# Kernel tuning notes

Hardware: AMD Instinct MI355X
Metric: run time of the kernel (lower is better)

The kernel has to match this reference:

```python
import jax, jax.numpy as jnp
import numpy as np

DIM = 1024
NUM_HEADS = 16
HEAD_DIM = DIM // NUM_HEADS
THETA = 10000.0


def apply_rope(x):
    # x: [B, S, H, D]; Llama-style interleaved rotary pairs.
    S, D = x.shape[1], x.shape[3]
    half = D // 2
    inv_freq = THETA ** (-jnp.arange(half, dtype=jnp.float32) * 2.0 / D)  # [D/2]
    angles = jnp.arange(S, dtype=jnp.float32)[:, None] * inv_freq[None, :]  # [S, D/2]
    cos = jnp.cos(angles)[None, :, None, :]  # [1,S,1,D/2]
    sin = jnp.sin(angles)[None, :, None, :]
    x_even = x[..., 0::2]
    x_odd = x[..., 1::2]
    out_even = x_even * cos - x_odd * sin
    out_odd = x_even * sin + x_odd * cos
    out = jnp.stack([out_even, out_odd], axis=-1).reshape(x.shape)
    return out.astype(x.dtype)


def setup_inputs() -> dict:
    key = jax.random.key(0)
    ks = jax.random.split(key, 5)
    B, S = 2, 2048
    x = jax.random.normal(ks[0], (B, S, DIM), dtype=jnp.float32)
    scale = 1.0 / np.sqrt(DIM)
    Wq = jax.random.normal(ks[1], (DIM, DIM), dtype=jnp.float32) * scale
    Wk = jax.random.normal(ks[2], (DIM, DIM), dtype=jnp.float32) * scale
    Wv = jax.random.normal(ks[3], (DIM, DIM), dtype=jnp.float32) * scale
    Wo = jax.random.normal(ks[4], (DIM, DIM), dtype=jnp.float32) * scale
    return {"x": x, "Wq": Wq, "Wk": Wk, "Wv": Wv, "Wo": Wo}


def reference(x, Wq, Wk, Wv, Wo):
    B, S, _ = x.shape
    # torch Linear: y = x @ W^T
    q = (x @ Wq.T).reshape(B, S, NUM_HEADS, HEAD_DIM)
    k = (x @ Wk.T).reshape(B, S, NUM_HEADS, HEAD_DIM)
    v = (x @ Wv.T).reshape(B, S, NUM_HEADS, HEAD_DIM)
    q = apply_rope(q)
    k = apply_rope(k)
    # causal SDPA, scale = 1/sqrt(head_dim)
    scale = 1.0 / np.sqrt(HEAD_DIM).astype(np.float32)
    scores = jnp.einsum("bqhd,bkhd->bhqk", q, k) * scale  # [B,H,S,S]
    causal = jnp.tril(jnp.ones((S, S), dtype=bool))
    scores = jnp.where(causal[None, None], scores, jnp.finfo(scores.dtype).min)
    attn = jax.nn.softmax(scores, axis=-1)
    y = jnp.einsum("bhqk,bkhd->bqhd", attn, v).reshape(B, S, DIM)
    return y @ Wo.T
```

## Files before the change

### kernel.cpp

```cpp
#include <hip/hip_runtime.h>
#include <hip/hip_bf16.h>

typedef __attribute__((ext_vector_type(8))) __bf16 bf16x8;
typedef __attribute__((ext_vector_type(4))) __bf16 bf16x4;
typedef __attribute__((ext_vector_type(4))) float f32x4;
typedef __attribute__((ext_vector_type(16))) float f32x16;
typedef __attribute__((ext_vector_type(2))) unsigned int uint2v;
typedef __attribute__((ext_vector_type(4))) unsigned int uint4v;

#define DIM 1024
#define SLEN 2048
#define NH 16
#define HD 64

__device__ __forceinline__ f32x4 MFMA(bf16x8 a, bf16x8 b, f32x4 c) {
    return __builtin_amdgcn_mfma_f32_16x16x32_bf16(a, b, c, 0, 0, 0);
}
__device__ __forceinline__ f32x16 MFMA32(bf16x8 a, bf16x8 b, f32x16 c) {
    return __builtin_amdgcn_mfma_f32_32x32x16_bf16(a, b, c, 0, 0, 0);
}
__device__ __forceinline__ unsigned cvtpk(float a, float b) {
    unsigned r;
    asm("v_cvt_pk_bf16_f32 %0, %1, %2" : "=v"(r) : "v"(a), "v"(b));
    return r;
}

__global__ __launch_bounds__(256) void cvt_all(const float* __restrict__ x,
                                               const float* __restrict__ w0,
                                               const float* __restrict__ w1,
                                               const float* __restrict__ w2,
                                               const float* __restrict__ w3,
                                               __bf16* __restrict__ xb,
                                               __bf16* __restrict__ o0,
                                               __bf16* __restrict__ o1,
                                               __bf16* __restrict__ o2,
                                               __bf16* __restrict__ o3) {
    const int s = blockIdx.y;
    const float* in;
    __bf16* out;
    if (s < 4) {
        in = x + (size_t)s * 1048576;
        out = xb + (size_t)s * 1048576;
    } else {
        in = s == 4 ? w0 : s == 5 ? w1 : s == 6 ? w2 : w3;
        out = s == 4 ? o0 : s == 5 ? o1 : s == 6 ? o2 : o3;
    }
    int i = (blockIdx.x * blockDim.x + threadIdx.x) * 8;
    f32x4 a = *reinterpret_cast<const f32x4*>(in + i);
    f32x4 b = *reinterpret_cast<const f32x4*>(in + i + 4);
    bf16x8 o;
#pragma unroll
    for (int j = 0; j < 4; ++j) { o[j] = (__bf16)a[j]; o[j + 4] = (__bf16)b[j]; }
    *reinterpret_cast<bf16x8*>(out + i) = o;
}

__global__ __launch_bounds__(256) void rope2v(__bf16* __restrict__ q,
                                              __bf16* __restrict__ k) {
    __bf16* t = blockIdx.y == 0 ? q : k;
    const float scale = blockIdx.y == 0 ? 0.18033688011112042f : 1.0f;
    const int idx = blockIdx.x * blockDim.x + threadIdx.x;
    const size_t o = (size_t)idx * 8;
    const int row = (int)(o >> 10);
    const int s = row & (SLEN - 1);
    const int jb = (int)(o & 63) >> 1;
    bf16x8 v = *reinterpret_cast<const bf16x8*>(t + o);
    bf16x8 r;
#pragma unroll
    for (int u = 0; u < 4; ++u) {
        const int j = jb + u;
        float inv = expf(-0.28782313662425574f * (float)j);
        float sn, cs;
        sincosf((float)s * inv, &sn, &cs);
        float e = (float)v[2 * u], od = (float)v[2 * u + 1];
        r[2 * u] = (__bf16)((e * cs - od * sn) * scale);
        r[2 * u + 1] = (__bf16)((e * sn + od * cs) * scale);
    }
    *reinterpret_cast<bf16x8*>(t + o) = r;
}

__global__ __launch_bounds__(256) void gemm_qkv(const __bf16* __restrict__ X,
                                                const __bf16* __restrict__ Wq,
                                                const __bf16* __restrict__ Wk,
                                                const __bf16* __restrict__ Wv,
                                                __bf16* __restrict__ Qo,
                                                __bf16* __restrict__ Ko,
                                                __bf16* __restrict__ Vt) {
    __shared__ alignas(16) __bf16 Alds[128 * 64];
    __shared__ alignas(16) __bf16 Blds[128 * 64];
    const int tid = threadIdx.x;
    const int lane = tid & 63;
    const int w = tid >> 6;
    const int wr = w >> 1, wc = w & 1;
    const int l15 = lane & 15, lhi = lane >> 4;
    const int l7 = l15 & 7;

    const int id = blockIdx.x;
    const int xcd = id & 7, j5 = id >> 3;
    const int m0 = ((xcd >> 1) * 8 + (j5 & 7)) * 128;
    const int n0g = ((xcd & 1) * 12 + (j5 >> 3)) * 128;
    const int seg = n0g >> 10;
    const int n0 = n0g & 1023;
    const __bf16* __restrict__ B = seg == 0 ? Wq : seg == 1 ? Wk : Wv;
    const int K = 1024, N = 1024;

    const int lrow = lane >> 3;
    const int scol = ((lane & 7) ^ lrow) * 8;

    f32x4 acc[4][4] = {};

    for (int kt = 0; kt < K; kt += 64) {
#pragma unroll
        for (int c = 0; c < 4; ++c) {
            int r0 = c * 32 + w * 8;
            const __bf16* sa = &X[(size_t)(m0 + r0 + lrow) * K + kt + scol];
            const __bf16* sb = &B[(size_t)(n0 + r0 + lrow) * K + kt + scol];
            __builtin_amdgcn_global_load_lds((const __attribute__((address_space(1))) void*)sa,
                                             (__attribute__((address_space(3))) void*)&Alds[r0 * 64],
                                             16, 0, 0);
            __builtin_amdgcn_global_load_lds((const __attribute__((address_space(1))) void*)sb,
                                             (__attribute__((address_space(3))) void*)&Blds[r0 * 64],
                                             16, 0, 0);
        }
        __syncthreads();
#pragma unroll
        for (int kk = 0; kk < 2; ++kk) {
            bf16x8 af[4], bfr[4];
#pragma unroll
            for (int i = 0; i < 4; ++i) {
                af[i] = *(const bf16x8*)&Alds[(wr * 64 + i * 16 + l15) * 64 + 8 * ((kk * 4 + lhi) ^ l7)];
                bfr[i] = *(const bf16x8*)&Blds[(wc * 64 + i * 16 + l15) * 64 + 8 * ((kk * 4 + lhi) ^ l7)];
            }
            __builtin_amdgcn_s_setprio(1);
#pragma unroll
            for (int i = 0; i < 4; ++i)
#pragma unroll
                for (int j = 0; j < 4; ++j)
                    acc[i][j] = MFMA(af[i], bfr[j], acc[i][j]);
            __builtin_amdgcn_s_setprio(0);
        }
        __syncthreads();
    }
    if (seg < 2) {
        __bf16* __restrict__ O = seg == 0 ? Qo : Ko;
#pragma unroll
        for (int i = 0; i < 4; ++i)
#pragma unroll
            for (int j = 0; j < 4; ++j)
#pragma unroll
                for (int r = 0; r < 4; ++r) {
                    int row = m0 + wr * 64 + i * 16 + lhi * 4 + r;
                    int col = n0 + wc * 64 + j * 16 + l15;
                    O[(size_t)row * N + col] = (__bf16)acc[i][j][r];
                }
    } else {
#pragma unroll
        for (int i = 0; i < 4; ++i)
#pragma unroll
            for (int j = 0; j < 4; ++j) {
                int row = m0 + wr * 64 + i * 16 + lhi * 4;
                int col = n0 + wc * 64 + j * 16 + l15;
                int bb = row >> 11, s = row & 2047;
                int hh = col >> 6, d = col & 63;
                bf16x4 pk;
#pragma unroll
                for (int r = 0; r < 4; ++r) pk[r] = (__bf16)acc[i][j][r];
                *(bf16x4*)&Vt[((size_t)(bb * 16 + hh) * 64 + d) * SLEN + s] = pk;
            }
    }
}

__global__ __launch_bounds__(256) void gemm_o(const __bf16* __restrict__ A,
                                              const __bf16* __restrict__ B,
                                              float* __restrict__ C) {
    __shared__ alignas(16) __bf16 Alds[64 * 64];
    __shared__ alignas(16) __bf16 Blds[128 * 64];
    const int tid = threadIdx.x;
    const int lane = tid & 63;
    const int w = tid >> 6;
    const int wr = w >> 1, wc = w & 1;
    const int l15 = lane & 15, lhi = lane >> 4;
    const int l7 = l15 & 7;

    const int id = blockIdx.x;
    const int xcd = id & 7, j5 = id >> 3;
    const int m0 = ((xcd >> 1) * 16 + (j5 & 15)) * 64;
    const int n0 = ((xcd & 1) * 4 + (j5 >> 4)) * 128;
    const int K = 1024, N = 1024;

    const int lrow = lane >> 3;
    const int scol = ((lane & 7) ^ lrow) * 8;

    f32x4 acc[2][4] = {};

    for (int kt = 0; kt < K; kt += 64) {
#pragma unroll
        for (int c = 0; c < 2; ++c) {
            int r0 = c * 32 + w * 8;
            const __bf16* sa = &A[(size_t)(m0 + r0 + lrow) * K + kt + scol];
            __builtin_amdgcn_global_load_lds((const __attribute__((address_space(1))) void*)sa,
                                             (__attribute__((address_space(3))) void*)&Alds[r0 * 64],
                                             16, 0, 0);
        }
#pragma unroll
        for (int c = 0; c < 4; ++c) {
            int r0 = c * 32 + w * 8;
            const __bf16* sb = &B[(size_t)(n0 + r0 + lrow) * K + kt + scol];
            __builtin_amdgcn_global_load_lds((const __attribute__((address_space(1))) void*)sb,
                                             (__attribute__((address_space(3))) void*)&Blds[r0 * 64],
                                             16, 0, 0);
        }
        __syncthreads();
#pragma unroll
        for (int kk = 0; kk < 2; ++kk) {
            bf16x8 af[2], bfr[4];
#pragma unroll
            for (int i = 0; i < 2; ++i)
                af[i] = *(const bf16x8*)&Alds[(wr * 32 + i * 16 + l15) * 64 + 8 * ((kk * 4 + lhi) ^ l7)];
#pragma unroll
            for (int j = 0; j < 4; ++j)
                bfr[j] = *(const bf16x8*)&Blds[(wc * 64 + j * 16 + l15) * 64 + 8 * ((kk * 4 + lhi) ^ l7)];
            __builtin_amdgcn_s_setprio(1);
#pragma unroll
            for (int i = 0; i < 2; ++i)
#pragma unroll
                for (int j = 0; j < 4; ++j)
                    acc[i][j] = MFMA(af[i], bfr[j], acc[i][j]);
            __builtin_amdgcn_s_setprio(0);
        }
        __syncthreads();
    }
#pragma unroll
    for (int i = 0; i < 2; ++i)
#pragma unroll
        for (int j = 0; j < 4; ++j)
#pragma unroll
            for (int r = 0; r < 4; ++r) {
                int row = m0 + wr * 32 + i * 16 + lhi * 4 + r;
                int col = n0 + wc * 64 + j * 16 + l15;
                C[(size_t)row * N + col] = acc[i][j][r];
            }
}

__global__ __launch_bounds__(256, 4) void attn_kernel(const __bf16* __restrict__ Q,
                                                      const __bf16* __restrict__ K,
                                                      const __bf16* __restrict__ Vt,
                                                      __bf16* __restrict__ Y) {
    __shared__ __bf16 Klds[2][64 * 64];
    __shared__ __bf16 Vlds[2][64 * 64];

    const int tid = threadIdx.x;
    const int lane = tid & 63;
    const int w = tid >> 6;
    const int qhalf = w & 1, khalf = w >> 1;
    const int l31 = lane & 31;
    const int hi32 = lane >> 5;
    const int l7 = l31 & 7;

    const int id = blockIdx.x;
    const int x = id & 7, jj = id >> 3;
    const int qi = jj >> 2;
    const int g = qi >> 3, r = qi & 7;
    const int qt = g == 0 ? 31 - r : g == 1 ? r : g == 2 ? 23 - r : 8 + r;
    const int bh = 4 * x + (jj & 3);
    const int b = bh >> 4, h = bh & 15;

    const int srow = lane >> 3;
    const int scs = (lane & 7) ^ srow;
    const __bf16* skP = K + (size_t)b * SLEN * DIM + h * HD + (size_t)(8 * w + srow) * DIM + scs * 8;
    const __bf16* svP = Vt + (size_t)bh * 64 * SLEN + (size_t)(8 * w + srow) * SLEN + scs * 8;
    const int dA = (8 * w + srow) * 64;

    auto stage = [&](int buf) {
#pragma unroll
        for (int i = 0; i < 2; ++i) {
            __builtin_amdgcn_global_load_lds(
                (const __attribute__((address_space(1))) void*)(skP + (size_t)i * 32 * DIM),
                (__attribute__((address_space(3))) void*)&Klds[buf][dA + i * 32 * 64], 16, 0, 0);
            __builtin_amdgcn_global_load_lds(
                (const __attribute__((address_space(1))) void*)(svP + (size_t)i * 32 * SLEN),
                (__attribute__((address_space(3))) void*)&Vlds[buf][dA + i * 32 * 64], 16, 0, 0);
        }
        skP += 64 * DIM;
        svP += 64;
    };

    const int qloc = qhalf * 32 + l31;
    const int qg = qt * 64 + qloc;
    const size_t qbase = (size_t)(b * SLEN + qg) * DIM + h * HD;
    bf16x8 qf0 = *(const bf16x8*)&Q[qbase + 0 + 8 * hi32];
    bf16x8 qf1 = *(const bf16x8*)&Q[qbase + 16 + 8 * hi32];
    bf16x8 qf2 = *(const bf16x8*)&Q[qbase + 32 + 8 * hi32];
    bf16x8 qf3 = *(const bf16x8*)&Q[qbase + 48 + 8 * hi32];

    const int krowbase = (khalf * 32 + l31) * 64;
    const int koff0 = krowbase + 8 * ((0 + hi32) ^ l7);
    const int koff1 = krowbase + 8 * ((2 + hi32) ^ l7);
    const int koff2 = krowbase + 8 * ((4 + hi32) ^ l7);
    const int koff3 = krowbase + 8 * ((6 + hi32) ^ l7);
    const int vrow0 = l31 * 64, vrow1 = (32 + l31) * 64;
    const int voff00 = vrow0 + 8 * ((4 * khalf + 0 + hi32) ^ l7);
    const int voff01 = vrow0 + 8 * ((4 * khalf + 2 + hi32) ^ l7);
    const int voff10 = vrow1 + 8 * ((4 * khalf + 0 + hi32) ^ l7);
    const int voff11 = vrow1 + 8 * ((4 * khalf + 2 + hi32) ^ l7);

    bf16x8 ones;
#pragma unroll
    for (int t = 0; t < 8; ++t) ones[t] = (__bf16)1.0f;

    f32x16 acc0 = {}, acc1 = {};
    f32x16 accL = {};

    const int nkt = qt + 1;
    stage(0);
    for (int kt = 0; kt < nkt; ++kt) {
        const int cur = kt & 1;
        __syncthreads();
        if (kt + 1 < nkt) stage(cur ^ 1);
        const __bf16* Kc = Klds[cur];
        const __bf16* Vc = Vlds[cur];

        f32x16 S = {};
        __builtin_amdgcn_s_setprio(1);
        S = MFMA32(*(const bf16x8*)&Kc[koff0], qf0, S);
        S = MFMA32(*(const bf16x8*)&Kc[koff1], qf1, S);
        S = MFMA32(*(const bf16x8*)&Kc[koff2], qf2, S);
        S = MFMA32(*(const bf16x8*)&Kc[koff3], qf3, S);
        __builtin_amdgcn_s_setprio(0);

        if (kt == qt) {
#pragma unroll
            for (int r2 = 0; r2 < 16; ++r2) {
                const int krow = (r2 & 3) + 8 * (r2 >> 2) + 4 * hi32 + 32 * khalf;
                if (krow > qloc) S[r2] = -1e30f;
            }
        }
        float p[16];
#pragma unroll
        for (int r2 = 0; r2 < 16; ++r2) p[r2] = exp2f(S[r2]);

        bf16x8 pf[2];
#pragma unroll
        for (int ss = 0; ss < 2; ++ss) {
            unsigned P01 = cvtpk(p[8 * ss + 0], p[8 * ss + 1]);
            unsigned P23 = cvtpk(p[8 * ss + 2], p[8 * ss + 3]);
            unsigned Q01 = cvtpk(p[8 * ss + 4], p[8 * ss + 5]);
            unsigned Q23 = cvtpk(p[8 * ss + 6], p[8 * ss + 7]);
            uint2v sa = __builtin_amdgcn_permlane32_swap(P01, Q01, false, false);
            uint2v sb = __builtin_amdgcn_permlane32_swap(P23, Q23, false, false);
            uint4v pwv = {sa[0], sb[0], sa[1], sb[1]};
            pf[ss] = __builtin_bit_cast(bf16x8, pwv);
        }

        __builtin_amdgcn_s_setprio(1);
        accL = MFMA32(ones, pf[0], accL);
        accL = MFMA32(ones, pf[1], accL);
        acc0 = MFMA32(*(const bf16x8*)&Vc[voff00], pf[0], acc0);
        acc0 = MFMA32(*(const bf16x8*)&Vc[voff01], pf[1], acc0);
        acc1 = MFMA32(*(const bf16x8*)&Vc[voff10], pf[0], acc1);
        acc1 = MFMA32(*(const bf16x8*)&Vc[voff11], pf[1], acc1);
        __builtin_amdgcn_s_setprio(0);
    }

    float lsum = accL[0];
    float* fbuf = (float*)&Klds[0][0];
    float* lbuf = (float*)&Vlds[0][0];
    __syncthreads();
    if (khalf == 1) {
#pragma unroll
        for (int r2 = 0; r2 < 16; ++r2) {
            fbuf[(qhalf * 2 + 0) * 1024 + r2 * 64 + lane] = acc0[r2];
            fbuf[(qhalf * 2 + 1) * 1024 + r2 * 64 + lane] = acc1[r2];
        }
        lbuf[qhalf * 64 + lane] = lsum;
    }
    __syncthreads();
    if (khalf == 0) {
#pragma unroll
        for (int r2 = 0; r2 < 16; ++r2) {
            acc0[r2] += fbuf[(qhalf * 2 + 0) * 1024 + r2 * 64 + lane];
            acc1[r2] += fbuf[(qhalf * 2 + 1) * 1024 + r2 * 64 + lane];
        }
        lsum += lbuf[qhalf * 64 + lane];
        const float inv = 1.0f / lsum;
        const size_t obase = (size_t)(b * SLEN + qg) * DIM + h * HD;
#pragma unroll
        for (int gg = 0; gg < 4; ++gg) {
            bf16x4 o0, o1;
#pragma unroll
            for (int e = 0; e < 4; ++e) {
                o0[e] = (__bf16)(acc0[gg * 4 + e] * inv);
                o1[e] = (__bf16)(acc1[gg * 4 + e] * inv);
            }
            *(bf16x4*)&Y[obase + 8 * gg + 4 * hi32] = o0;
            *(bf16x4*)&Y[obase + 32 + 8 * gg + 4 * hi32] = o1;
        }
    }
}

extern "C" void kernel_launch(void* const* d_in, const int* in_sizes, int n_in,
                              void* d_out, int out_size, void* d_ws, size_t ws_size,
                              hipStream_t stream) {
    const float* x = (const float*)d_in[0];
    const float* Wq = (const float*)d_in[1];
    const float* Wk = (const float*)d_in[2];
    const float* Wv = (const float*)d_in[3];
    const float* Wo = (const float*)d_in[4];
    float* out = (float*)d_out;

    const size_t XN = (size_t)4096 * 1024;
    const size_t WN = (size_t)1024 * 1024;

    __bf16* xb = (__bf16*)d_ws;
    __bf16* qb = xb + XN;
    __bf16* kb = qb + XN;
    __bf16* vtb = kb + XN;
    __bf16* wqb = vtb + XN;
    __bf16* wkb = wqb + WN;
    __bf16* wvb = wkb + WN;
    __bf16* wob = wvb + WN;
    __bf16* yb = xb;

    dim3 gc(512, 8);
    cvt_all<<<gc, 256, 0, stream>>>(x, Wq, Wk, Wv, Wo, xb, wqb, wkb, wvb, wob);

    gemm_qkv<<<768, 256, 0, stream>>>(xb, wqb, wkb, wvb, qb, kb, vtb);

    dim3 gr(2048, 2);
    rope2v<<<gr, 256, 0, stream>>>(qb, kb);

    attn_kernel<<<1024, 256, 0, stream>>>(qb, kb, vtb, yb);

    gemm_o<<<512, 256, 0, stream>>>(yb, wob, out);
}
```

Measured before the change: 103.4 us.

## Enlarge attention query tile to 128 rows with 512-thread blocks

The attention kernel now processes 128 query rows per block with 8 waves (4 query quads x 2 key halves), halving the grid and sharing each staged K/V tile across twice as many queries. Staging uses one async load per thread per tile. Causal masking and skipping are made per-wave, so waves whose query range ends before a key tile skip its compute. This aims to reduce redundant K/V global traffic, at the cost of fewer blocks, a coarser causal schedule and some idle waves on diagonal tiles.

After: 110.3 us. 1.07x slower.

```diff
diff --git a/kernel.cpp b/kernel.cpp
--- a/kernel.cpp
+++ b/kernel.cpp
@@ -241,51 +241,47 @@
             }
 }
 
-__global__ __launch_bounds__(256, 4) void attn_kernel(const __bf16* __restrict__ Q,
+__global__ __launch_bounds__(512, 4) void attn_kernel(const __bf16* __restrict__ Q,
                                                       const __bf16* __restrict__ K,
                                                       const __bf16* __restrict__ Vt,
                                                       __bf16* __restrict__ Y) {
     __shared__ __bf16 Klds[2][64 * 64];
     __shared__ __bf16 Vlds[2][64 * 64];
+    __shared__ float lsmall[4][64];
 
     const int tid = threadIdx.x;
     const int lane = tid & 63;
     const int w = tid >> 6;
-    const int qhalf = w & 1, khalf = w >> 1;
+    const int qquad = w & 3, khalf = w >> 2;
     const int l31 = lane & 31;
     const int hi32 = lane >> 5;
     const int l7 = l31 & 7;
 
     const int id = blockIdx.x;
     const int x = id & 7, jj = id >> 3;
-    const int qi = jj >> 2;
-    const int g = qi >> 3, r = qi & 7;
-    const int qt = g == 0 ? 31 - r : g == 1 ? r : g == 2 ? 23 - r : 8 + r;
+    const int qt = (jj < 32) ? (15 - (jj >> 2)) : ((jj - 32) >> 2);
     const int bh = 4 * x + (jj & 3);
     const int b = bh >> 4, h = bh & 15;
 
-    const int srow = lane >> 3;
-    const int scs = (lane & 7) ^ srow;
-    const __bf16* skP = K + (size_t)b * SLEN * DIM + h * HD + (size_t)(8 * w + srow) * DIM + scs * 8;
-    const __bf16* svP = Vt + (size_t)bh * 64 * SLEN + (size_t)(8 * w + srow) * SLEN + scs * 8;
-    const int dA = (8 * w + srow) * 64;
+    const int srow = tid >> 3;
+    const int scs = ((tid & 7) ^ (srow & 7)) * 8;
+    const __bf16* skP = K + (size_t)(b * SLEN + srow) * DIM + h * HD + scs;
+    const __bf16* svP = Vt + (size_t)(bh * 64 + srow) * SLEN + scs;
+    const int dA = srow * 64;
 
     auto stage = [&](int buf) {
-#pragma unroll
-        for (int i = 0; i < 2; ++i) {
-            __builtin_amdgcn_global_load_lds(
-                (const __attribute__((address_space(1))) void*)(skP + (size_t)i * 32 * DIM),
-                (__attribute__((address_space(3))) void*)&Klds[buf][dA + i * 32 * 64], 16, 0, 0);
-            __builtin_amdgcn_global_load_lds(
-                (const __attribute__((address_space(1))) void*)(svP + (size_t)i * 32 * SLEN),
-                (__attribute__((address_space(3))) void*)&Vlds[buf][dA + i * 32 * 64], 16, 0, 0);
-        }
-        skP += 64 * DIM;
+        __builtin_amdgcn_global_load_lds(
+            (const __attribute__((address_space(1))) void*)skP,
+            (__attribute__((address_space(3))) void*)&Klds[buf][dA], 16, 0, 0);
+        __builtin_amdgcn_global_load_lds(
+            (const __attribute__((address_space(1))) void*)svP,
+            (__attribute__((address_space(3))) void*)&Vlds[buf][dA], 16, 0, 0);
+        skP += (size_t)64 * DIM;
         svP += 64;
     };
 
-    const int qloc = qhalf * 32 + l31;
-    const int qg = qt * 64 + qloc;
+    const int qloc = qquad * 32 + l31;
+    const int qg = qt * 128 + qloc;
     const size_t qbase = (size_t)(b * SLEN + qg) * DIM + h * HD;
     bf16x8 qf0 = *(const bf16x8*)&Q[qbase + 0 + 8 * hi32];
     bf16x8 qf1 = *(const bf16x8*)&Q[qbase + 16 + 8 * hi32];
@@ -310,12 +306,14 @@
     f32x16 acc0 = {}, acc1 = {};
     f32x16 accL = {};
 
-    const int nkt = qt + 1;
+    const int nkt = 2 * qt + 2;
+    const int skipAbove = qt * 128 + qquad * 32 + 31;
     stage(0);
     for (int kt = 0; kt < nkt; ++kt) {
         const int cur = kt & 1;
         __syncthreads();
         if (kt + 1 < nkt) stage(cur ^ 1);
+        if (kt * 64 > skipAbove) continue;
         const __bf16* Kc = Klds[cur];
         const __bf16* Vc = Vlds[cur];
 
@@ -327,11 +325,11 @@
         S = MFMA32(*(const bf16x8*)&Kc[koff3], qf3, S);
         __builtin_amdgcn_s_setprio(0);
 
-        if (kt == qt) {
+        if (kt * 64 + 63 > qt * 128 + qquad * 32) {
 #pragma unroll
             for (int r2 = 0; r2 < 16; ++r2) {
-                const int krow = (r2 & 3) + 8 * (r2 >> 2) + 4 * hi32 + 32 * khalf;
-                if (krow > qloc) S[r2] = -1e30f;
+                const int key = kt * 64 + (r2 & 3) + 8 * (r2 >> 2) + 4 * hi32 + 32 * khalf;
+                if (key > qg) S[r2] = -1e30f;
             }
         }
         float p[16];
@@ -362,25 +360,25 @@
     }
 
     float lsum = accL[0];
-    float* fbuf = (float*)&Klds[0][0];
-    float* lbuf = (float*)&Vlds[0][0];
+    float* fbuf0 = (float*)&Klds[0][0];
+    float* fbuf1 = (float*)&Vlds[0][0];
     __syncthreads();
     if (khalf == 1) {
 #pragma unroll
         for (int r2 = 0; r2 < 16; ++r2) {
-            fbuf[(qhalf * 2 + 0) * 1024 + r2 * 64 + lane] = acc0[r2];
-            fbuf[(qhalf * 2 + 1) * 1024 + r2 * 64 + lane] = acc1[r2];
-        }
-        lbuf[qhalf * 64 + lane] = lsum;
+            fbuf0[qquad * 1024 + r2 * 64 + lane] = acc0[r2];
+            fbuf1[qquad * 1024 + r2 * 64 + lane] = acc1[r2];
+        }
+        lsmall[qquad][lane] = lsum;
     }
     __syncthreads();
     if (khalf == 0) {
 #pragma unroll
         for (int r2 = 0; r2 < 16; ++r2) {
-            acc0[r2] += fbuf[(qhalf * 2 + 0) * 1024 + r2 * 64 + lane];
-            acc1[r2] += fbuf[(qhalf * 2 + 1) * 1024 + r2 * 64 + lane];
-        }
-        lsum += lbuf[qhalf * 64 + lane];
+            acc0[r2] += fbuf0[qquad * 1024 + r2 * 64 + lane];
+            acc1[r2] += fbuf1[qquad * 1024 + r2 * 64 + lane];
+        }
+        lsum += lsmall[qquad][lane];
         const float inv = 1.0f / lsum;
         const size_t obase = (size_t)(b * SLEN + qg) * DIM + h * HD;
 #pragma unroll
@@ -428,7 +426,7 @@
     dim3 gr(2048, 2);
     rope2v<<<gr, 256, 0, stream>>>(qb, kb);
 
-    attn_kernel<<<1024, 256, 0, stream>>>(qb, kb, vtb, yb);
+    attn_kernel<<<512, 512, 0, stream>>>(qb, kb, vtb, yb);
 
     gemm_o<<<512, 256, 0, stream>>>(yb, wob, out);
 }
```
